# Performance work log

Measured on AMD Instinct MI355X. Metric: run time of the kernel, lower is better.

The kernel has to match this reference:

```python
import jax, jax.numpy as jnp
import numpy as np

V, T, L, CE, WE, H, NTAG, PAD = 100000, 65536, 16, 15, 15, 30, 45, 84


def setup_inputs() -> dict:
    key = jax.random.key(0)
    ks = jax.random.split(key, 16)
    s = 0.1
    return {
        "word_ids": jax.random.randint(ks[0], (T,), 0, V, dtype=jnp.int32),
        "char_ids": jax.random.randint(ks[1], (T, L), 0, 85, dtype=jnp.int32),
        "word_lens": jax.random.randint(ks[2], (T,), 1, L + 1, dtype=jnp.int32),
        "wordEmbeds": jax.random.normal(ks[3], (V, WE), jnp.float32) * s,
        "charEmbeds": jax.random.normal(ks[4], (85, CE), jnp.float32) * s,
        "conv_w": jax.random.normal(ks[5], (CE, 3 * CE), jnp.float32) * s,  # Conv1d(1,15,45) flattened
        "conv_b": jax.random.normal(ks[6], (CE,), jnp.float32) * s,
        "wih_f": jax.random.normal(ks[7], (4 * H, 2 * WE), jnp.float32) * s,
        "whh_f": jax.random.normal(ks[8], (4 * H, H), jnp.float32) * s,
        "bih_f": jax.random.normal(ks[9], (4 * H,), jnp.float32) * s,
        "bhh_f": jnp.zeros((4 * H,), jnp.float32),
        "wih_b": jax.random.normal(ks[10], (4 * H, 2 * WE), jnp.float32) * s,
        "whh_b": jax.random.normal(ks[11], (4 * H, H), jnp.float32) * s,
        "bih_b": jax.random.normal(ks[12], (4 * H,), jnp.float32) * s,
        "bhh_b": jnp.zeros((4 * H,), jnp.float32),
        "lin_w": jax.random.normal(ks[13], (NTAG, 2 * H), jnp.float32) * s,
        "lin_b": jax.random.normal(ks[14], (NTAG,), jnp.float32) * s,
    }


def _char_features(char_ids, word_lens, charEmbeds, conv_w, conv_b):
    # replicate original: neighbor idx valid iff 0 < idx < len(word), else PAD char 84
    pos = jnp.arange(L)
    nidx = pos[:, None] + jnp.array([-1, 0, 1])  # [L,3]
    valid = (nidx[None] > 0) & (nidx[None] < word_lens[:, None, None])  # [T,L,3]
    gidx = jnp.clip(nidx, 0, L - 1).reshape(-1)  # [L*3]
    cids = char_ids[:, gidx].reshape(-1, L, 3)
    cids = jnp.where(valid, cids, PAD)
    win = charEmbeds[cids].reshape(-1, L, 3 * CE)  # [T,L,45]
    feat = jnp.einsum("tlk,fk->tlf", win, conv_w) + conv_b  # [T,L,15]
    mask = pos[None, :] < word_lens[:, None]  # maxpool over word length only
    feat = jnp.where(mask[:, :, None], feat, -jnp.inf)
    return feat.max(axis=1)  # [T,15]


def _lstm_dir(x, Wih, Whh, bih, bhh):
    def step(carry, xt):
        h, c = carry
        g = xt @ Wih.T + bih + h @ Whh.T + bhh
        i, f, gg, o = jnp.split(g, 4)
        c = jax.nn.sigmoid(f) * c + jax.nn.sigmoid(i) * jnp.tanh(gg)
        h = jax.nn.sigmoid(o) * jnp.tanh(c)
        return (h, c), h
    z = jnp.zeros((H,), x.dtype)
    _, hs = jax.lax.scan(step, (z, z), x)
    return hs


def reference(word_ids, char_ids, word_lens, wordEmbeds, charEmbeds, conv_w, conv_b,
              wih_f, whh_f, bih_f, bhh_f, wih_b, whh_b, bih_b, bhh_b, lin_w, lin_b):
    cf = _char_features(char_ids, word_lens, charEmbeds, conv_w, conv_b)
    x = jnp.concatenate([wordEmbeds[word_ids], cf], axis=-1)  # [T,30]
    hf = _lstm_dir(x, wih_f, whh_f, bih_f, bhh_f)
    hb = _lstm_dir(x[::-1], wih_b, whh_b, bih_b, bhh_b)[::-1]
    out = jnp.concatenate([hf, hb], axis=-1)  # [T,60]
    logits = out @ lin_w.T + lin_b  # [T,45]
    return jax.nn.softmax(logits, axis=-1)
```

## Files before the change

### kernel.cpp

```cpp
#include <hip/hip_runtime.h>
#include <hip/hip_bf16.h>
#include <hip/hip_fp16.h>
#include <math.h>

#define T_TOK 65536
#define L_CH  16
#define CE_D  15
#define WE_D  15
#define HDIM  30
#define NTAG  45
#define PADC  84
#define NCHR  85
#define PFD   4
#define CL    32
#define WU    16
#define XPAD  16
#define NCHUNK (T_TOK / CL)
#define PSTRIDE 52
#define PSZ   (NCHR * PSTRIDE)

#define SC_SIG  (-1.44269504089f)
#define SC_TANH ( 2.88539008178f)

typedef float v2f __attribute__((ext_vector_type(2)));
typedef float v4f __attribute__((ext_vector_type(4)));

__device__ __forceinline__ float frcp(float x) { return __builtin_amdgcn_rcpf(x); }
__device__ __forceinline__ float fexp2(float x) { return __builtin_amdgcn_exp2f(x); }
__device__ __forceinline__ v2f fma2(v2f a, v2f b, v2f c) { return __builtin_elementwise_fma(a, b, c); }

__device__ __forceinline__ float dpp_xor1(float x) {
    int r = __builtin_amdgcn_mov_dpp(__float_as_int(x), 0xB1, 0xF, 0xF, true);
    return __int_as_float(r);
}

__global__ __launch_bounds__(256) void setup_kernel(
    const float* __restrict__ charEmbeds, const float* __restrict__ conv_w,
    const float* __restrict__ conv_b, float* __restrict__ P_g,
    unsigned int* __restrict__ xgF_alloc, unsigned int* __restrict__ xgB_alloc)
{
    for (int i = threadIdx.x; i < XPAD * 64; i += 256) {
        xgF_alloc[i] = 0u; xgF_alloc[(size_t)(XPAD + T_TOK) * 64 + i] = 0u;
        xgB_alloc[i] = 0u; xgB_alloc[(size_t)(XPAD + T_TOK) * 64 + i] = 0u;
    }

    for (int idx = threadIdx.x; idx < NCHR * 45; idx += 256) {
        int c = idx / 45, r = idx - c * 45;
        int k = r / 15, f = r - k * 15;
        float acc = (k == 1) ? conv_b[f] : 0.f;
        #pragma unroll
        for (int e = 0; e < CE_D; e++)
            acc = fmaf(charEmbeds[c * CE_D + e], conv_w[f * 45 + k * 15 + e], acc);
        P_g[c * PSTRIDE + k * 16 + f] = acc;
    }
    for (int idx = threadIdx.x; idx < NCHR * 3; idx += 256) {
        int c = idx / 3, k = idx - c * 3;
        P_g[c * PSTRIDE + k * 16 + 15] = 0.f;
    }
}

__global__ __launch_bounds__(256, 3) void build_fused_kernel(
    const int* __restrict__ word_ids, const int* __restrict__ char_ids,
    const int* __restrict__ word_lens, const float* __restrict__ wordEmbeds,
    const float* __restrict__ P_g,
    const float* __restrict__ wihF, const float* __restrict__ bihF, const float* __restrict__ bhhF,
    const float* __restrict__ wihB, const float* __restrict__ bihB, const float* __restrict__ bhhB,
    unsigned int* __restrict__ xgF_alloc, unsigned int* __restrict__ xgB_alloc)
{
    __shared__ __align__(16) float sP[PSZ];
    __shared__ __align__(16) float sX[128 * 36];

    const int tb = blockIdx.x * 128;

    for (int i = threadIdx.x; i < PSZ; i += 256) sP[i] = P_g[i];
    __syncthreads();

    if (threadIdx.x < 128) {
        int t = tb + threadIdx.x;
        int wl = word_lens[t];
        const int4* cr4 = (const int4*)(char_ids + (size_t)t * L_CH);
        int4 q0 = cr4[0], q1 = cr4[1], q2 = cr4[2], q3 = cr4[3];
        int c[16] = { q0.x, q0.y, q0.z, q0.w, q1.x, q1.y, q1.z, q1.w,
                      q2.x, q2.y, q2.z, q2.w, q3.x, q3.y, q3.z, q3.w };

        v4f cf4[4];
        #pragma unroll
        for (int q = 0; q < 4; q++) cf4[q] = (v4f){-INFINITY, -INFINITY, -INFINITY, -INFINITY};

        #pragma unroll
        for (int l = 0; l < 16; l++) {
            if (l < wl) {
                int c0 = (l >= 2) ? c[l - 1] : PADC;
                int c1 = (l >= 1) ? c[l] : PADC;
                int c2 = (l < 15) ? ((l + 1 < wl) ? c[l + 1] : PADC) : PADC;
                const v4f* p0 = (const v4f*)&sP[c0 * PSTRIDE];
                const v4f* p1 = (const v4f*)&sP[c1 * PSTRIDE + 16];
                const v4f* p2 = (const v4f*)&sP[c2 * PSTRIDE + 32];
                #pragma unroll
                for (int q = 0; q < 4; q++) {
                    v4f s = (p0[q] + p1[q]) + p2[q];
                    cf4[q] = __builtin_elementwise_max(cf4[q], s);
                }
            }
        }

        int wid = word_ids[t];
        const float* we = wordEmbeds + (size_t)wid * WE_D;
        float cfa[16];
        #pragma unroll
        for (int q = 0; q < 4; q++) *(v4f*)&cfa[4 * q] = cf4[q];
        float xo[32];
        #pragma unroll
        for (int e = 0; e < WE_D; e++) xo[e] = we[e];
        #pragma unroll
        for (int m = 0; m < CE_D; m++) xo[WE_D + m] = cfa[m];
        xo[30] = 0.f; xo[31] = 0.f;
        float* dst = &sX[threadIdx.x * 36];
        #pragma unroll
        for (int q = 0; q < 8; q++) *(float4*)&dst[4 * q] = ((const float4*)xo)[q];
    }
    __syncthreads();

    const int w = threadIdx.x >> 6;
    const int l = threadIdx.x & 63;
    const int u = l >> 1, sub = l & 1;

    int ra = sub ? 30 + u : u;
    int rb = sub ? 90 + u : 60 + u;
    if (u >= 30) { ra = 0; rb = 0; }
    const float scA = SC_SIG;
    const float scB = sub ? SC_SIG : SC_TANH;

    v2f wAF[16], wBF[16], wAB[16], wBB[16];
    {
        const float2* pAF = (const float2*)(wihF + ra * 30);
        const float2* pBF = (const float2*)(wihF + rb * 30);
        const float2* pAB = (const float2*)(wihB + ra * 30);
        const float2* pBB = (const float2*)(wihB + rb * 30);
        #pragma unroll
        for (int j = 0; j < 15; j++) {
            float2 a = pAF[j], b = pBF[j], cA = pAB[j], d = pBB[j];
            wAF[j] = (v2f){a.x * scA, a.y * scA};
            wBF[j] = (v2f){b.x * scB, b.y * scB};
            wAB[j] = (v2f){cA.x * scA, cA.y * scA};
            wBB[j] = (v2f){d.x * scB, d.y * scB};
        }
        wAF[15] = (v2f){0.f, 0.f}; wBF[15] = (v2f){0.f, 0.f};
        wAB[15] = (v2f){0.f, 0.f}; wBB[15] = (v2f){0.f, 0.f};
    }
    const float bAF = (bihF[ra] + bhhF[ra]) * scA;
    const float bBF = (bihF[rb] + bhhF[rb]) * scB;
    const float bAB = (bihB[ra] + bhhB[ra]) * scA;
    const float bBB = (bihB[rb] + bhhB[rb]) * scB;

    const int tt0 = w * 32;
    #pragma unroll 1
    for (int tt = tt0; tt < tt0 + 32; tt++) {
        const v4f* xp4 = (const v4f*)&sX[tt * 36];
        v2f aF0 = {bAF, 0.f}, aF1 = {0.f, 0.f}, bF0 = {bBF, 0.f}, bF1 = {0.f, 0.f};
        v2f aB0 = {bAB, 0.f}, aB1 = {0.f, 0.f}, bB0 = {bBB, 0.f}, bB1 = {0.f, 0.f};
        #pragma unroll
        for (int kk = 0; kk < 4; kk++) {
            v4f xA = xp4[2 * kk], xB = xp4[2 * kk + 1];
            v2f xa = {xA.x, xA.y}, xb = {xA.z, xA.w};
            v2f xc = {xB.x, xB.y}, xd = {xB.z, xB.w};
            aF0 = fma2(wAF[4 * kk],     xa, aF0); aF1 = fma2(wAF[4 * kk + 1], xb, aF1);
            bF0 = fma2(wBF[4 * kk],     xa, bF0); bF1 = fma2(wBF[4 * kk + 1], xb, bF1);
            aB0 = fma2(wAB[4 * kk],     xa, aB0); aB1 = fma2(wAB[4 * kk + 1], xb, aB1);
            bB0 = fma2(wBB[4 * kk],     xa, bB0); bB1 = fma2(wBB[4 * kk + 1], xb, bB1);
            aF0 = fma2(wAF[4 * kk + 2], xc, aF0); aF1 = fma2(wAF[4 * kk + 3], xd, aF1);
            bF0 = fma2(wBF[4 * kk + 2], xc, bF0); bF1 = fma2(wBF[4 * kk + 3], xd, bF1);
            aB0 = fma2(wAB[4 * kk + 2], xc, aB0); aB1 = fma2(wAB[4 * kk + 3], xd, aB1);
            bB0 = fma2(wBB[4 * kk + 2], xc, bB0); bB1 = fma2(wBB[4 * kk + 3], xd, bB1);
        }
        float aF = (aF0.x + aF1.x) + (aF0.y + aF1.y);
        float bF = (bF0.x + bF1.x) + (bF0.y + bF1.y);
        float aB = (aB0.x + aB1.x) + (aB0.y + aB1.y);
        float bB = (bB0.x + bB1.x) + (bB0.y + bB1.y);
        __half2 pkF = __floats2half2_rn(aF, bF);
        __half2 pkB = __floats2half2_rn(aB, bB);
        unsigned int oF = (u < 30) ? *(unsigned int*)&pkF : 0u;
        unsigned int oB = (u < 30) ? *(unsigned int*)&pkB : 0u;
        int t = tb + tt;
        xgF_alloc[(size_t)(XPAD + t) * 64 + l] = oF;
        xgB_alloc[(size_t)(XPAD + t) * 64 + l] = oB;
    }
}

__global__ __launch_bounds__(64, 2) void lstm_kernel(
    const float* __restrict__ whhF, const float* __restrict__ whhB,
    const unsigned int* __restrict__ xgF,
    const unsigned int* __restrict__ xgB,
    const float* __restrict__ lin_w, const float* __restrict__ lin_b,
    float* __restrict__ out)
{
    __shared__ __align__(16) float h_bcF[32];
    __shared__ __align__(16) float h_bcB[32];
    __shared__ float sH[2][CL][33];
    __shared__ float sW[NTAG * 60];
    __shared__ float sB[NTAG];

    const int chunk = blockIdx.x;
    const int l = threadIdx.x;
    const int u = l >> 1, sub = l & 1;

    for (int i = threadIdx.x; i < NTAG * 60; i += 64) sW[i] = lin_w[i];
    if (threadIdx.x < NTAG) sB[threadIdx.x] = lin_b[threadIdx.x];

    if (l < 32) { h_bcF[l] = 0.f; h_bcB[l] = 0.f; }
    const int wl30 = (!sub) && (u < 30);

    int ra = sub ? 30 + u : u;
    int rb = sub ? 90 + u : 60 + u;
    if (u >= 30) { ra = 0; rb = 0; }
    const float scA = SC_SIG;
    const float scB = sub ? SC_SIG : SC_TANH;

    v2f waF[16], wbF[16], waB[16], wbB[16];
    {
        const float2* pAF = (const float2*)(whhF + ra * 30);
        const float2* pBF = (const float2*)(whhF + rb * 30);
        const float2* pAB = (const float2*)(whhB + ra * 30);
        const float2* pBB = (const float2*)(whhB + rb * 30);
        #pragma unroll
        for (int j = 0; j < 15; j++) {
            float2 a = pAF[j], b = pBF[j], cA = pAB[j], d = pBB[j];
            waF[j] = (v2f){a.x * scA, a.y * scA};
            wbF[j] = (v2f){b.x * scB, b.y * scB};
            waB[j] = (v2f){cA.x * scA, cA.y * scA};
            wbB[j] = (v2f){d.x * scB, d.y * scB};
        }
        waF[15] = (v2f){0.f, 0.f}; wbF[15] = (v2f){0.f, 0.f};
        waB[15] = (v2f){0.f, 0.f}; wbB[15] = (v2f){0.f, 0.f};
    }

    const float Aa = sub ? 0.f : 1.f;
    const float Bb = sub ? 1.f : -2.f;

    const int cstart = chunk * CL;
    const int cend = cstart + CL;
    const int sbegF = cstart - WU;
    const int sbegB = cend - 1 + WU;

    float hF = 0.f, ccF = 0.f, hB = 0.f, ccB = 0.f;
    unsigned int bufF[PFD], bufB[PFD];
    #pragma unroll
    for (int d = 0; d < PFD; d++) {
        bufF[d] = xgF[(long)(sbegF + d) * 64 + l];
        bufB[d] = xgB[(long)(sbegB - d) * 64 + l];
    }
    const unsigned int* ppfF = xgF + (long)(sbegF + PFD) * 64 + l;
    const unsigned int* ppfB = xgB + (long)(sbegB - PFD) * 64 + l;

    const v2f* hlF = (const v2f*)h_bcF;
    const v2f* hlB = (const v2f*)h_bcB;

    auto STEP = [&](int d, int doStore, int srowF) {
        unsigned int gFbits = bufF[d]; bufF[d] = *ppfF; ppfF += 64;
        unsigned int gBbits = bufB[d]; bufB[d] = *ppfB; ppfB -= 64;
        __half2 ghF = *(__half2*)&gFbits;
        __half2 ghB = *(__half2*)&gBbits;

        v2f aF0 = {__low2float(ghF), 0.f}, aF1 = {0.f, 0.f};
        v2f bF0 = {__high2float(ghF), 0.f}, bF1 = {0.f, 0.f};
        v2f aB0 = {__low2float(ghB), 0.f}, aB1 = {0.f, 0.f};
        v2f bB0 = {__high2float(ghB), 0.f}, bB1 = {0.f, 0.f};
        #pragma unroll
        for (int kk = 0; kk < 4; kk++) {
            v2f fa = hlF[4 * kk],     fb = hlF[4 * kk + 1];
            v2f fc = hlF[4 * kk + 2], fd = hlF[4 * kk + 3];
            v2f ba = hlB[4 * kk],     bb = hlB[4 * kk + 1];
            v2f bc = hlB[4 * kk + 2], bd = hlB[4 * kk + 3];
            aF0 = fma2(waF[4 * kk],     fa, aF0); aF1 = fma2(waF[4 * kk + 1], fb, aF1);
            bF0 = fma2(wbF[4 * kk],     fa, bF0); bF1 = fma2(wbF[4 * kk + 1], fb, bF1);
            aB0 = fma2(waB[4 * kk],     ba, aB0); aB1 = fma2(waB[4 * kk + 1], bb, aB1);
            bB0 = fma2(wbB[4 * kk],     ba, bB0); bB1 = fma2(wbB[4 * kk + 1], bb, bB1);
            aF0 = fma2(waF[4 * kk + 2], fc, aF0); aF1 = fma2(waF[4 * kk + 3], fd, aF1);
            bF0 = fma2(wbF[4 * kk + 2], fc, bF0); bF1 = fma2(wbF[4 * kk + 3], fd, bF1);
            aB0 = fma2(waB[4 * kk + 2], bc, aB0); aB1 = fma2(waB[4 * kk + 3], bd, aB1);
            bB0 = fma2(wbB[4 * kk + 2], bc, bB0); bB1 = fma2(wbB[4 * kk + 3], bd, bB1);
        }
        float accF0 = (aF0.x + aF1.x) + (aF0.y + aF1.y);
        float accF1 = (bF0.x + bF1.x) + (bF0.y + bF1.y);
        float accB0 = (aB0.x + aB1.x) + (aB0.y + aB1.y);
        float accB1 = (bB0.x + bB1.x) + (bB0.y + bB1.y);

        float r0F = frcp(1.f + fexp2(accF0));
        float r1F = fmaf(Bb, frcp(1.f + fexp2(accF1)), Aa);
        float r0B = frcp(1.f + fexp2(accB0));
        float r1B = fmaf(Bb, frcp(1.f + fexp2(accB1)), Aa);

        float s0F = dpp_xor1(r0F), s1F = dpp_xor1(r1F);
        float s0B = dpp_xor1(r0B), s1B = dpp_xor1(r1B);
        float ivF = sub ? s0F : r0F, fvF = sub ? r0F : s0F;
        float gvF = sub ? s1F : r1F, ovF = sub ? r1F : s1F;
        float ivB = sub ? s0B : r0B, fvB = sub ? r0B : s0B;
        float gvB = sub ? s1B : r1B, ovB = sub ? r1B : s1B;

        ccF = fmaf(fvF, ccF, ivF * gvF);
        ccB = fmaf(fvB, ccB, ivB * gvB);
        float thF = fmaf(-2.f, frcp(1.f + fexp2(SC_TANH * ccF)), 1.f);
        float thB = fmaf(-2.f, frcp(1.f + fexp2(SC_TANH * ccB)), 1.f);
        hF = ovF * thF;
        hB = ovB * thB;

        if (wl30) { h_bcF[u] = hF; h_bcB[u] = hB; }
        if (doStore && wl30) {
            sH[0][srowF][u] = hF;
            sH[1][CL - 1 - srowF][u] = hB;
        }
    };

    #pragma unroll 1
    for (int s = 0; s < WU; s += PFD) {
        STEP(0, 0, 0); STEP(1, 0, 0); STEP(2, 0, 0); STEP(3, 0, 0);
    }
    #pragma unroll 1
    for (int s = 0; s < CL; s += PFD) {
        STEP(0, 1, s + 0); STEP(1, 1, s + 1); STEP(2, 1, s + 2); STEP(3, 1, s + 3);
    }

    __syncthreads();
    const int tloc = l >> 1;
    const int q = l & 1;
    const int kb = q ? 23 : 0;
    const int nt = q ? 22 : 23;

    float hx[60];
    #pragma unroll
    for (int j = 0; j < 30; j++) { hx[j] = sH[0][tloc][j]; hx[30 + j] = sH[1][tloc][j]; }

    float lg[23];
    float mx = -INFINITY;
    #pragma unroll
    for (int i = 0; i < 23; i++) {
        if (i < nt) {
            int k = kb + i;
            float acc = sB[k];
            const float* wv = &sW[k * 60];
            #pragma unroll
            for (int j = 0; j < 60; j++) acc = fmaf(hx[j], wv[j], acc);
            lg[i] = acc;
            mx = fmaxf(mx, acc);
        } else lg[i] = -INFINITY;
    }
    mx = fmaxf(mx, dpp_xor1(mx));
    float sum = 0.f;
    #pragma unroll
    for (int i = 0; i < 23; i++) { lg[i] = __expf(lg[i] - mx); sum += lg[i]; }
    sum += dpp_xor1(sum);
    float inv = frcp(sum);
    float* op = out + (size_t)(cstart + tloc) * NTAG + kb;
    for (int i = 0; i < nt; i++) op[i] = lg[i] * inv;
}

extern "C" void kernel_launch(void* const* d_in, const int* in_sizes, int n_in,
                              void* d_out, int out_size, void* d_ws, size_t ws_size,
                              hipStream_t stream)
{
    const int*   word_ids   = (const int*)d_in[0];
    const int*   char_ids   = (const int*)d_in[1];
    const int*   word_lens  = (const int*)d_in[2];
    const float* wordEmbeds = (const float*)d_in[3];
    const float* charEmbeds = (const float*)d_in[4];
    const float* conv_w     = (const float*)d_in[5];
    const float* conv_b     = (const float*)d_in[6];
    const float* wih_f      = (const float*)d_in[7];
    const float* whh_f      = (const float*)d_in[8];
    const float* bih_f      = (const float*)d_in[9];
    const float* bhh_f      = (const float*)d_in[10];
    const float* wih_b      = (const float*)d_in[11];
    const float* whh_b      = (const float*)d_in[12];
    const float* bih_b      = (const float*)d_in[13];
    const float* bhh_b      = (const float*)d_in[14];
    const float* lin_w      = (const float*)d_in[15];
    const float* lin_b      = (const float*)d_in[16];
    float* out = (float*)d_out;

    unsigned int* xgF_alloc = (unsigned int*)d_ws;
    unsigned int* xgB_alloc = xgF_alloc + (size_t)(T_TOK + 2 * XPAD) * 64;
    float* P_g = (float*)(xgB_alloc + (size_t)(T_TOK + 2 * XPAD) * 64);

    setup_kernel<<<1, 256, 0, stream>>>(charEmbeds, conv_w, conv_b, P_g, xgF_alloc, xgB_alloc);

    build_fused_kernel<<<T_TOK / 128, 256, 0, stream>>>(
        word_ids, char_ids, word_lens, wordEmbeds, P_g,
        wih_f, bih_f, bhh_f, wih_b, bih_b, bhh_b, xgF_alloc, xgB_alloc);

    lstm_kernel<<<NCHUNK, 64, 0, stream>>>(
        whh_f, whh_b,
        xgF_alloc + (size_t)XPAD * 64, xgB_alloc + (size_t)XPAD * 64,
        lin_w, lin_b, out);
}
```

Before: 104.4 us.

## Remap LSTM lanes so each computes all gates, and halve the chunk length

The recurrent kernel now gives each half of the wavefront one direction. Each lane computes all four gates for one hidden unit, so the DPP gate exchange between lane pairs goes away and the per-step FMA chain gets shorter. The chunk length drops from 32 to 16 tokens, which doubles the number of blocks, and occupancy is raised to 3 waves per SIMD. In exchange, the fixed 16-step warmup now costs more relative to the useful steps, and the projection/softmax is spread over 4 lanes per token.

```diff
diff --git a/kernel.cpp b/kernel.cpp
--- a/kernel.cpp
+++ b/kernel.cpp
@@ -12,9 +12,9 @@
 #define PADC  84
 #define NCHR  85
 #define PFD   4
-#define CL    32
+#define CL    16
 #define WU    16
-#define XPAD  16
+#define XPAD  20
 #define NCHUNK (T_TOK / CL)
 #define PSTRIDE 52
 #define PSZ   (NCHR * PSTRIDE)
@@ -31,6 +31,10 @@
 
 __device__ __forceinline__ float dpp_xor1(float x) {
     int r = __builtin_amdgcn_mov_dpp(__float_as_int(x), 0xB1, 0xF, 0xF, true);
+    return __int_as_float(r);
+}
+__device__ __forceinline__ float dpp_xor2(float x) {
+    int r = __builtin_amdgcn_mov_dpp(__float_as_int(x), 0x4E, 0xF, 0xF, true);
     return __int_as_float(r);
 }
 
@@ -187,155 +191,131 @@
     }
 }
 
-__global__ __launch_bounds__(64, 2) void lstm_kernel(
+__global__ __launch_bounds__(64, 3) void lstm_kernel(
     const float* __restrict__ whhF, const float* __restrict__ whhB,
     const unsigned int* __restrict__ xgF,
     const unsigned int* __restrict__ xgB,
     const float* __restrict__ lin_w, const float* __restrict__ lin_b,
     float* __restrict__ out)
 {
-    __shared__ __align__(16) float h_bcF[32];
-    __shared__ __align__(16) float h_bcB[32];
+    __shared__ __align__(16) float h_bc[68];
     __shared__ float sH[2][CL][33];
     __shared__ float sW[NTAG * 60];
     __shared__ float sB[NTAG];
 
     const int chunk = blockIdx.x;
+    const int cstart = chunk * CL;
     const int l = threadIdx.x;
-    const int u = l >> 1, sub = l & 1;
-
-    for (int i = threadIdx.x; i < NTAG * 60; i += 64) sW[i] = lin_w[i];
-    if (threadIdx.x < NTAG) sB[threadIdx.x] = lin_b[threadIdx.x];
-
-    if (l < 32) { h_bcF[l] = 0.f; h_bcB[l] = 0.f; }
-    const int wl30 = (!sub) && (u < 30);
-
-    int ra = sub ? 30 + u : u;
-    int rb = sub ? 90 + u : 60 + u;
-    if (u >= 30) { ra = 0; rb = 0; }
-    const float scA = SC_SIG;
-    const float scB = sub ? SC_SIG : SC_TANH;
-
-    v2f waF[16], wbF[16], waB[16], wbB[16];
+    const int half = l >> 5;
+    const int u = l & 31;
+    const int uu = (u < 30) ? u : 0;
+    const int active = (u < 30);
+
+    for (int i = l; i < NTAG * 60; i += 64) sW[i] = lin_w[i];
+    if (l < NTAG) sB[l] = lin_b[l];
+
+    h_bc[half * 34 + u] = 0.f;
+
+    const float* whh = half ? whhB : whhF;
+    v2f wi2[15], wf2[15], wg2[15], wo2[15];
     {
-        const float2* pAF = (const float2*)(whhF + ra * 30);
-        const float2* pBF = (const float2*)(whhF + rb * 30);
-        const float2* pAB = (const float2*)(whhB + ra * 30);
-        const float2* pBB = (const float2*)(whhB + rb * 30);
+        const float2* pi = (const float2*)(whh + (size_t)uu * 30);
+        const float2* pf = (const float2*)(whh + (size_t)(30 + uu) * 30);
+        const float2* pg = (const float2*)(whh + (size_t)(60 + uu) * 30);
+        const float2* po = (const float2*)(whh + (size_t)(90 + uu) * 30);
         #pragma unroll
         for (int j = 0; j < 15; j++) {
-            float2 a = pAF[j], b = pBF[j], cA = pAB[j], d = pBB[j];
-            waF[j] = (v2f){a.x * scA, a.y * scA};
-            wbF[j] = (v2f){b.x * scB, b.y * scB};
-            waB[j] = (v2f){cA.x * scA, cA.y * scA};
-            wbB[j] = (v2f){d.x * scB, d.y * scB};
-        }
-        waF[15] = (v2f){0.f, 0.f}; wbF[15] = (v2f){0.f, 0.f};
-        waB[15] = (v2f){0.f, 0.f}; wbB[15] = (v2f){0.f, 0.f};
-    }
-
-    const float Aa = sub ? 0.f : 1.f;
-    const float Bb = sub ? 1.f : -2.f;
-
-    const int cstart = chunk * CL;
-    const int cend = cstart + CL;
-    const int sbegF = cstart - WU;
-    const int sbegB = cend - 1 + WU;
-
-    float hF = 0.f, ccF = 0.f, hB = 0.f, ccB = 0.f;
-    unsigned int bufF[PFD], bufB[PFD];
+            float2 a = pi[j], b = pf[j], g = pg[j], o = po[j];
+            wi2[j] = (v2f){a.x * SC_SIG,  a.y * SC_SIG};
+            wf2[j] = (v2f){b.x * SC_SIG,  b.y * SC_SIG};
+            wg2[j] = (v2f){g.x * SC_TANH, g.y * SC_TANH};
+            wo2[j] = (v2f){o.x * SC_SIG,  o.y * SC_SIG};
+        }
+    }
+
+    const unsigned int* pp = half ? (xgB + (long)(cstart + CL - 1 + WU) * 64 + 2 * u)
+                                  : (xgF + (long)(cstart - WU) * 64 + 2 * u);
+    const long sdir = half ? -64 : 64;
+    uint2 buf[PFD];
     #pragma unroll
-    for (int d = 0; d < PFD; d++) {
-        bufF[d] = xgF[(long)(sbegF + d) * 64 + l];
-        bufB[d] = xgB[(long)(sbegB - d) * 64 + l];
-    }
-    const unsigned int* ppfF = xgF + (long)(sbegF + PFD) * 64 + l;
-    const unsigned int* ppfB = xgB + (long)(sbegB - PFD) * 64 + l;
-
-    const v2f* hlF = (const v2f*)h_bcF;
-    const v2f* hlB = (const v2f*)h_bcB;
-
-    auto STEP = [&](int d, int doStore, int srowF) {
-        unsigned int gFbits = bufF[d]; bufF[d] = *ppfF; ppfF += 64;
-        unsigned int gBbits = bufB[d]; bufB[d] = *ppfB; ppfB -= 64;
-        __half2 ghF = *(__half2*)&gFbits;
-        __half2 ghB = *(__half2*)&gBbits;
-
-        v2f aF0 = {__low2float(ghF), 0.f}, aF1 = {0.f, 0.f};
-        v2f bF0 = {__high2float(ghF), 0.f}, bF1 = {0.f, 0.f};
-        v2f aB0 = {__low2float(ghB), 0.f}, aB1 = {0.f, 0.f};
-        v2f bB0 = {__high2float(ghB), 0.f}, bB1 = {0.f, 0.f};
-        #pragma unroll
-        for (int kk = 0; kk < 4; kk++) {
-            v2f fa = hlF[4 * kk],     fb = hlF[4 * kk + 1];
-            v2f fc = hlF[4 * kk + 2], fd = hlF[4 * kk + 3];
-            v2f ba = hlB[4 * kk],     bb = hlB[4 * kk + 1];
-            v2f bc = hlB[4 * kk + 2], bd = hlB[4 * kk + 3];
-            aF0 = fma2(waF[4 * kk],     fa, aF0); aF1 = fma2(waF[4 * kk + 1], fb, aF1);
-            bF0 = fma2(wbF[4 * kk],     fa, bF0); bF1 = fma2(wbF[4 * kk + 1], fb, bF1);
-            aB0 = fma2(waB[4 * kk],     ba, aB0); aB1 = fma2(waB[4 * kk + 1], bb, aB1);
-            bB0 = fma2(wbB[4 * kk],     ba, bB0); bB1 = fma2(wbB[4 * kk + 1], bb, bB1);
-            aF0 = fma2(waF[4 * kk + 2], fc, aF0); aF1 = fma2(waF[4 * kk + 3], fd, aF1);
-            bF0 = fma2(wbF[4 * kk + 2], fc, bF0); bF1 = fma2(wbF[4 * kk + 3], fd, bF1);
-            aB0 = fma2(waB[4 * kk + 2], bc, aB0); aB1 = fma2(waB[4 * kk + 3], bd, aB1);
-            bB0 = fma2(wbB[4 * kk + 2], bc, bB0); bB1 = fma2(wbB[4 * kk + 3], bd, bB1);
-        }
-        float accF0 = (aF0.x + aF1.x) + (aF0.y + aF1.y);
-        float accF1 = (bF0.x + bF1.x) + (bF0.y + bF1.y);
-        float accB0 = (aB0.x + aB1.x) + (aB0.y + aB1.y);
-        float accB1 = (bB0.x + bB1.x) + (bB0.y + bB1.y);
-
-        float r0F = frcp(1.f + fexp2(accF0));
-        float r1F = fmaf(Bb, frcp(1.f + fexp2(accF1)), Aa);
-        float r0B = frcp(1.f + fexp2(accB0));
-        float r1B = fmaf(Bb, frcp(1.f + fexp2(accB1)), Aa);
-
-        float s0F = dpp_xor1(r0F), s1F = dpp_xor1(r1F);
-        float s0B = dpp_xor1(r0B), s1B = dpp_xor1(r1B);
-        float ivF = sub ? s0F : r0F, fvF = sub ? r0F : s0F;
-        float gvF = sub ? s1F : r1F, ovF = sub ? r1F : s1F;
-        float ivB = sub ? s0B : r0B, fvB = sub ? r0B : s0B;
-        float gvB = sub ? s1B : r1B, ovB = sub ? r1B : s1B;
-
-        ccF = fmaf(fvF, ccF, ivF * gvF);
-        ccB = fmaf(fvB, ccB, ivB * gvB);
-        float thF = fmaf(-2.f, frcp(1.f + fexp2(SC_TANH * ccF)), 1.f);
-        float thB = fmaf(-2.f, frcp(1.f + fexp2(SC_TANH * ccB)), 1.f);
-        hF = ovF * thF;
-        hB = ovB * thB;
-
-        if (wl30) { h_bcF[u] = hF; h_bcB[u] = hB; }
-        if (doStore && wl30) {
-            sH[0][srowF][u] = hF;
-            sH[1][CL - 1 - srowF][u] = hB;
+    for (int d = 0; d < PFD; d++) { buf[d] = *(const uint2*)pp; pp += sdir; }
+
+    float* sHp = &sH[half][half ? CL - 1 : 0][uu];
+    const long shinc = half ? -33 : 33;
+    const v2f* hl2 = (const v2f*)(h_bc + half * 34);
+
+    float h = 0.f, cc = 0.f;
+
+    auto STEP = [&](int d, int doStore) {
+        uint2 g2v = buf[d];
+        buf[d] = *(const uint2*)pp; pp += sdir;
+        __half2 pig = *(__half2*)&g2v.x;
+        __half2 pfo = *(__half2*)&g2v.y;
+
+        v2f ai0 = {__low2float(pig), 0.f},  ai1 = {0.f, 0.f};
+        v2f ag0 = {__high2float(pig), 0.f}, ag1 = {0.f, 0.f};
+        v2f af0 = {__low2float(pfo), 0.f},  af1 = {0.f, 0.f};
+        v2f ao0 = {__high2float(pfo), 0.f}, ao1 = {0.f, 0.f};
+        #pragma unroll
+        for (int j = 0; j < 7; j++) {
+            v2f h0 = hl2[j], h1 = hl2[j + 7];
+            ai0 = fma2(wi2[j], h0, ai0); ai1 = fma2(wi2[j + 7], h1, ai1);
+            af0 = fma2(wf2[j], h0, af0); af1 = fma2(wf2[j + 7], h1, af1);
+            ag0 = fma2(wg2[j], h0, ag0); ag1 = fma2(wg2[j + 7], h1, ag1);
+            ao0 = fma2(wo2[j], h0, ao0); ao1 = fma2(wo2[j + 7], h1, ao1);
+        }
+        {
+            v2f h14 = hl2[14];
+            ai0 = fma2(wi2[14], h14, ai0);
+            af0 = fma2(wf2[14], h14, af0);
+            ag0 = fma2(wg2[14], h14, ag0);
+            ao0 = fma2(wo2[14], h14, ao0);
+        }
+        float ai = (ai0.x + ai1.x) + (ai0.y + ai1.y);
+        float af = (af0.x + af1.x) + (af0.y + af1.y);
+        float ag = (ag0.x + ag1.x) + (ag0.y + ag1.y);
+        float ao = (ao0.x + ao1.x) + (ao0.y + ao1.y);
+
+        float ii = frcp(1.f + fexp2(ai));
+        float ff = frcp(1.f + fexp2(af));
+        float gg = fmaf(-2.f, frcp(1.f + fexp2(ag)), 1.f);
+        float oo = frcp(1.f + fexp2(ao));
+
+        cc = fmaf(ff, cc, ii * gg);
+        float th = fmaf(-2.f, frcp(1.f + fexp2(SC_TANH * cc)), 1.f);
+        h = oo * th;
+
+        if (active) h_bc[half * 34 + u] = h;
+        if (doStore) {
+            if (active) *sHp = h;
+            sHp += shinc;
         }
     };
 
     #pragma unroll 1
     for (int s = 0; s < WU; s += PFD) {
-        STEP(0, 0, 0); STEP(1, 0, 0); STEP(2, 0, 0); STEP(3, 0, 0);
+        STEP(0, 0); STEP(1, 0); STEP(2, 0); STEP(3, 0);
     }
     #pragma unroll 1
     for (int s = 0; s < CL; s += PFD) {
-        STEP(0, 1, s + 0); STEP(1, 1, s + 1); STEP(2, 1, s + 2); STEP(3, 1, s + 3);
+        STEP(0, 1); STEP(1, 1); STEP(2, 1); STEP(3, 1);
     }
 
     __syncthreads();
-    const int tloc = l >> 1;
-    const int q = l & 1;
-    const int kb = q ? 23 : 0;
-    const int nt = q ? 22 : 23;
+    const int tloc = l >> 2;
+    const int q = l & 3;
+    const int kb = q * 12;
 
     float hx[60];
     #pragma unroll
     for (int j = 0; j < 30; j++) { hx[j] = sH[0][tloc][j]; hx[30 + j] = sH[1][tloc][j]; }
 
-    float lg[23];
+    float lg[12];
     float mx = -INFINITY;
     #pragma unroll
-    for (int i = 0; i < 23; i++) {
-        if (i < nt) {
-            int k = kb + i;
+    for (int i = 0; i < 12; i++) {
+        int k = kb + i;
+        if (k < NTAG) {
             float acc = sB[k];
             const float* wv = &sW[k * 60];
             #pragma unroll
@@ -345,12 +325,15 @@
         } else lg[i] = -INFINITY;
     }
     mx = fmaxf(mx, dpp_xor1(mx));
+    mx = fmaxf(mx, dpp_xor2(mx));
     float sum = 0.f;
     #pragma unroll
-    for (int i = 0; i < 23; i++) { lg[i] = __expf(lg[i] - mx); sum += lg[i]; }
+    for (int i = 0; i < 12; i++) { lg[i] = __expf(lg[i] - mx); sum += lg[i]; }
     sum += dpp_xor1(sum);
+    sum += dpp_xor2(sum);
     float inv = frcp(sum);
     float* op = out + (size_t)(cstart + tloc) * NTAG + kb;
+    const int nt = (kb + 12 <= NTAG) ? 12 : (NTAG - kb);
     for (int i = 0; i < nt; i++) op[i] = lg[i] * inv;
 }
 
```

After: 231.8 us. +122.0%, slower.
